# Performance work log

Measured on AMD Instinct MI355X. Metric: run time of the kernel, lower is better.

Reference implementation:

```python
import jax, jax.numpy as jnp
import numpy as np

DIM = 256
HEADS = 8


def setup_inputs() -> dict:
    key = jax.random.key(0)
    ks = jax.random.split(key, 12)
    B, N, L, C, H = 2, 1024, 4096, DIM, HEADS
    s = C ** -0.5
    inp = {
        "query": jax.random.normal(ks[0], (B, N, C), jnp.float32),
        "key": jax.random.normal(ks[1], (B, L, C), jnp.float32),
        "value": jax.random.normal(ks[2], (B, L, C), jnp.float32),
        "key_padding_mask": jnp.zeros((B, L), jnp.bool_),
        "hw_lvl": 1,
        # nn.Linear weights, stored as (out, in) like torch
        "Wq": jax.random.normal(ks[3], (C, C), jnp.float32) * s,
        "Wk": jax.random.normal(ks[4], (C, C), jnp.float32) * s,
        "Wv": jax.random.normal(ks[5], (C, C), jnp.float32) * s,
        "Wp": jax.random.normal(ks[6], (C, C), jnp.float32) * s,
        "bp": jax.random.normal(ks[7], (C,), jnp.float32) * 0.02,
        "W1": jax.random.normal(ks[8], (H, H), jnp.float32) * H ** -0.5,
        "b1": jax.random.normal(ks[9], (H,), jnp.float32) * 0.02,
        "W2": jax.random.normal(ks[10], (1, H), jnp.float32) * H ** -0.5,
        "b2": jax.random.normal(ks[11], (1,), jnp.float32) * 0.02,
    }
    return inp


def reference(query, key, value, key_padding_mask, hw_lvl,
              Wq, Wk, Wv, Wp, bp, W1, b1, W2, b2):
    # key_padding_mask and hw_lvl are accepted but unused by the original module.
    B, N, C = query.shape
    L = key.shape[1]
    H = W1.shape[0]
    D = C // H
    scale = D ** -0.5

    q = (query @ Wq.T).reshape(B, N, H, D)  # bnhd
    k = (key @ Wk.T).reshape(B, L, H, D)    # blhd
    v = (value @ Wv.T).reshape(B, L, H, D)  # blhd

    # raw attention scores [B, H, N, L]
    attn = jnp.einsum("bnhd,blhd->bhnl", q, k) * scale

    # per-score tiny MLP over the head axis -> mask [B, N, L, 1]
    scores_nlh = attn.transpose(0, 2, 3, 1)  # [B, N, L, H]
    new_feats = jax.nn.relu(scores_nlh @ W1.T + b1)
    mask = jax.nn.relu(new_feats @ W2.T + b2)  # [B, N, L, 1]

    a = jax.nn.softmax(attn, axis=-1)  # dropout p=0 -> identity
    x = jnp.einsum("bhnl,blhd->bnhd", a, v).reshape(B, N, C)
    x = x @ Wp.T + bp
    return x, mask
```

## Files before the change

kernel.cpp:

```cpp
#include <hip/hip_runtime.h>

typedef unsigned short u16;
typedef unsigned int u32;
typedef __attribute__((ext_vector_type(8))) short bf16x8;
typedef __attribute__((ext_vector_type(4))) short bf16x4;
typedef __attribute__((ext_vector_type(4))) float f32x4;

#define QK_SCALE 0.17677669529663687f

__device__ inline float bf2f(u16 h) {
    u32 u = ((u32)h) << 16; float f; __builtin_memcpy(&f, &u, 4); return f;
}
__device__ inline u16 f2bf(float f) {
    u32 u; __builtin_memcpy(&u, &f, 4);
    u = u + 0x7fffu + ((u >> 16) & 1u);
    return (u16)(u >> 16);
}

__global__ __launch_bounds__(256) void cvt_all_kernel(
    const float* __restrict__ q, const float* __restrict__ k,
    const float* __restrict__ v,
    const float* __restrict__ Wq, const float* __restrict__ Wk,
    const float* __restrict__ Wv, const float* __restrict__ Wp,
    u16* __restrict__ qf, u16* __restrict__ kf, u16* __restrict__ vf,
    u16* __restrict__ wqb, u16* __restrict__ wkb, u16* __restrict__ wvb,
    u16* __restrict__ wpb)
{
    const int bx = blockIdx.x;
    const float* src; u16* dst; int base;
    if (bx < 256)       { src = q;  dst = qf;  base = bx; }
    else if (bx < 1280) { src = k;  dst = kf;  base = bx - 256; }
    else if (bx < 2304) { src = v;  dst = vf;  base = bx - 1280; }
    else if (bx < 2336) { src = Wq; dst = wqb; base = bx - 2304; }
    else if (bx < 2368) { src = Wk; dst = wkb; base = bx - 2336; }
    else if (bx < 2400) { src = Wv; dst = wvb; base = bx - 2368; }
    else                { src = Wp; dst = wpb; base = bx - 2400; }
    const int i = base * 2048 + threadIdx.x * 8;
    const f32x4 a = *(const f32x4*)(src + i);
    const f32x4 b = *(const f32x4*)(src + i + 4);
    bf16x8 o;
#pragma unroll
    for (int j = 0; j < 4; ++j) {
        o[j]     = (short)f2bf(a[j]);
        o[j + 4] = (short)f2bf(b[j]);
    }
    *(bf16x8*)(dst + i) = o;
}

__global__ __launch_bounds__(256) void proj_kernel(
    const u16* __restrict__ qf, const u16* __restrict__ kf,
    const u16* __restrict__ vf,
    const u16* __restrict__ wqb, const u16* __restrict__ wkb,
    const u16* __restrict__ wvb,
    u16* __restrict__ qb, u16* __restrict__ kb, u16* __restrict__ vt)
{
    const int bx = blockIdx.x;
    const u16 *X, *W; u16* outb; int m0, mode;
    if (bx < 128)      { X = qf; W = wqb; outb = qb; m0 = bx * 16; mode = 2; }
    else if (bx < 640) { X = kf; W = wkb; outb = kb; m0 = (bx - 128) * 16; mode = 0; }
    else               { X = vf; W = wvb; outb = vt; m0 = (bx - 640) * 16; mode = 1; }

    const int lane = threadIdx.x & 63;
    const int w = threadIdx.x >> 6;
    const int r = lane & 15, g = lane >> 4;
    const int c0 = blockIdx.y * 64 + w * 16;
    const u16* ap = X + (long)(m0 + r) * 256 + g * 8;
    const u16* bp = W + (long)(c0 + r) * 256 + g * 8;

    bf16x8 af[8], bf[8];
#pragma unroll
    for (int ks = 0; ks < 8; ++ks) af[ks] = *(const bf16x8*)(ap + ks * 32);
#pragma unroll
    for (int ks = 0; ks < 8; ++ks) bf[ks] = *(const bf16x8*)(bp + ks * 32);

    f32x4 acc = {0.f, 0.f, 0.f, 0.f};
#pragma unroll
    for (int ks = 0; ks < 8; ++ks)
        acc = __builtin_amdgcn_mfma_f32_16x16x32_bf16(af[ks], bf[ks], acc, 0, 0, 0);

    const int c = c0 + r;
    if (mode == 1) {
        const int m_ = m0 + g * 4;
        const int b = m_ >> 12, l = m_ & 4095;
        bf16x4 pk;
#pragma unroll
        for (int j = 0; j < 4; ++j) pk[j] = (short)f2bf(acc[j]);
        *(bf16x4*)(vt + (long)b * 1048576 + (long)(l >> 2) * 1024 + c * 4) = pk;
    } else {
#pragma unroll
        for (int j = 0; j < 4; ++j) {
            const int m = m0 + g * 4 + j;
            if (mode == 2) outb[(long)m * 256 + c] = f2bf(acc[j] * QK_SCALE);
            else           outb[(long)m * 256 + c] = f2bf(acc[j]);
        }
    }
}

__global__ __launch_bounds__(256, 2) void attn_split_kernel(
    const u16* __restrict__ qb, const u16* __restrict__ kb,
    const u16* __restrict__ vt,
    const float* __restrict__ W1, const float* __restrict__ b1,
    const float* __restrict__ W2, const float* __restrict__ b2,
    u16* __restrict__ Opart, float* __restrict__ stats,
    float* __restrict__ out)
{
    __shared__ float ored[4][8][2][2][16][4];
    __shared__ float rs[4][8][16];

    const int tid = threadIdx.x;
    const int w = tid >> 6, lane = tid & 63;
    const int r = lane & 15, g = lane >> 4;
    const int bid = blockIdx.x;
    const int cz = bid & 7;
    const int bi = bid >> 9;
    const int n0 = ((bid >> 3) & 63) * 16;

    float w1r[64], b1r[8], w2r[8];
#pragma unroll
    for (int i = 0; i < 64; ++i) w1r[i] = W1[i];
#pragma unroll
    for (int i = 0; i < 8; ++i) { b1r[i] = b1[i]; w2r[i] = W2[i]; }
    const float b2r = b2[0];

    bf16x8 qh[8];
    const long qbase = (long)(bi * 1024 + n0 + r) * 256 + g * 8;
#pragma unroll
    for (int h = 0; h < 8; ++h)
        qh[h] = *(const bf16x8*)(qb + qbase + h * 32);

    f32x4 oacc[8][2];
#pragma unroll
    for (int h = 0; h < 8; ++h)
#pragma unroll
        for (int c = 0; c < 2; ++c) oacc[h][c] = (f32x4){0.f, 0.f, 0.f, 0.f};
    float rsum[8];
#pragma unroll
    for (int h = 0; h < 8; ++h) rsum[h] = 0.f;

    bf16x8 kf[8];
    {
        const long kbb = (long)(bi * 4096 + cz * 512 + w * 16 + r) * 256 + g * 8;
#pragma unroll
        for (int h = 0; h < 8; ++h)
            kf[h] = *(const bf16x8*)(kb + kbb + h * 32);
    }

    for (int t = 0; t < 8; ++t) {
        const int l0 = cz * 512 + t * 64;

        f32x4 ss[8];
#pragma unroll
        for (int h = 0; h < 8; ++h) {
            f32x4 z = {0.f, 0.f, 0.f, 0.f};
            ss[h] = __builtin_amdgcn_mfma_f32_16x16x32_bf16(kf[h], qh[h], z, 0, 0, 0);
        }

        if (t < 7) {
            const long kbb = (long)(bi * 4096 + l0 + 64 + w * 16 + r) * 256 + g * 8;
#pragma unroll
            for (int h = 0; h < 8; ++h)
                kf[h] = *(const bf16x8*)(kb + kbb + h * 32);
        }

        bf16x4 vf[8][2];
        {
            const u16* vb = vt + (long)bi * 1048576 +
                            (long)((l0 >> 2) + w * 4 + g) * 1024;
#pragma unroll
            for (int h = 0; h < 8; ++h)
#pragma unroll
                for (int c = 0; c < 2; ++c)
                    vf[h][c] = *(const bf16x4*)(vb + (h * 32 + c * 16 + r) * 4);
        }

        {
            f32x4 mv4;
#pragma unroll
            for (int j = 0; j < 4; ++j) {
                float mv = b2r;
#pragma unroll
                for (int f = 0; f < 8; ++f) {
                    float ft = b1r[f];
#pragma unroll
                    for (int h = 0; h < 8; ++h)
                        ft = fmaf(ss[h][j], w1r[f * 8 + h], ft);
                    mv = fmaf(fmaxf(ft, 0.f), w2r[f], mv);
                }
                mv4[j] = fmaxf(mv, 0.f);
            }
            *(f32x4*)(out + 524288l + (long)(bi * 1024 + n0 + r) * 4096
                      + l0 + w * 16 + g * 4) = mv4;
        }

        bf16x4 pa[8];
#pragma unroll
        for (int h = 0; h < 8; ++h) {
            float e0 = __expf(ss[h][0] - 8.f);
            float e1 = __expf(ss[h][1] - 8.f);
            float e2 = __expf(ss[h][2] - 8.f);
            float e3 = __expf(ss[h][3] - 8.f);
            rsum[h] += (e0 + e1) + (e2 + e3);
            u32 u0, u1, u2, u3;
            __builtin_memcpy(&u0, &e0, 4); __builtin_memcpy(&u1, &e1, 4);
            __builtin_memcpy(&u2, &e2, 4); __builtin_memcpy(&u3, &e3, 4);
            u32 lohi[2];
            lohi[0] = (u0 >> 16) | (u1 & 0xFFFF0000u);
            lohi[1] = (u2 >> 16) | (u3 & 0xFFFF0000u);
            __builtin_memcpy(&pa[h], lohi, 8);
        }

#pragma unroll
        for (int h = 0; h < 8; ++h)
#pragma unroll
            for (int c = 0; c < 2; ++c)
                oacc[h][c] = __builtin_amdgcn_mfma_f32_16x16x16bf16_1k(
                    pa[h], vf[h][c], oacc[h][c], 0, 0, 0);
    }

#pragma unroll
    for (int h = 0; h < 8; ++h) {
        float v = rsum[h];
        v += __shfl_xor(v, 16);
        v += __shfl_xor(v, 32);
        if (g == 0) rs[w][h][r] = v;
    }
#pragma unroll
    for (int ph = 0; ph < 2; ++ph) {
        if ((g >> 1) == ph) {
#pragma unroll
            for (int h = 0; h < 8; ++h)
#pragma unroll
                for (int c = 0; c < 2; ++c)
                    *(f32x4*)&ored[w][h][c][g & 1][r][0] = oacc[h][c];
        }
        __syncthreads();
        if (ph == 0 && tid < 128) {
            const int h = tid >> 4, n = tid & 15;
            stats[((long)(bi * 8 + cz) * 8 + h) * 1024 + n0 + n] =
                rs[0][h][n] + rs[1][h][n] + rs[2][h][n] + rs[3][h][n];
        }
        {
            const int h = tid >> 5, c = (tid >> 4) & 1, rr = tid & 15;
#pragma unroll
            for (int g2 = 0; g2 < 2; ++g2)
#pragma unroll
                for (int j = 0; j < 4; ++j) {
                    const float val =
                        ored[0][h][c][g2][rr][j] + ored[1][h][c][g2][rr][j] +
                        ored[2][h][c][g2][rr][j] + ored[3][h][c][g2][rr][j];
                    const int n = (ph * 2 + g2) * 4 + j;
                    Opart[((long)(bi * 8 + cz) * 1024 + n0 + n) * 256
                          + h * 32 + c * 16 + rr] = f2bf(val);
                }
        }
        if (ph == 0) __syncthreads();
    }
}

__global__ __launch_bounds__(512) void reduce_kernel(
    const u16* __restrict__ Opart, const float* __restrict__ stats,
    const u16* __restrict__ wpb, const float* __restrict__ bp,
    float* __restrict__ out)
{
    __shared__ __align__(16) u16 xt[16 * 272];
    const int tid = threadIdx.x;
    const int bi = blockIdx.y, n0 = blockIdx.x * 16, bz = blockIdx.z;

    {
        const int n = tid >> 5, cg = tid & 31, h = cg >> 2;
        float S = 0.f, O[8];
#pragma unroll
        for (int k = 0; k < 8; ++k) O[k] = 0.f;
#pragma unroll
        for (int c = 0; c < 8; ++c) {
            S += stats[((long)(bi * 8 + c) * 8 + h) * 1024 + n0 + n];
            bf16x8 v0 = *(const bf16x8*)(Opart +
                ((long)(bi * 8 + c) * 1024 + n0 + n) * 256 + cg * 8);
#pragma unroll
            for (int k = 0; k < 8; ++k) O[k] += bf2f((u16)v0[k]);
        }
        const float inv = 1.f / S;
        bf16x8 pk;
#pragma unroll
        for (int k = 0; k < 8; ++k) pk[k] = (short)f2bf(O[k] * inv);
        *(bf16x8*)(&xt[n * 272 + cg * 8]) = pk;
    }
    __syncthreads();

    const int w = tid >> 6, lane = tid & 63;
    const int r = lane & 15, g = lane >> 4;
    bf16x8 a8[8];
#pragma unroll
    for (int ks = 0; ks < 8; ++ks)
        a8[ks] = *(const bf16x8*)(&xt[r * 272 + ks * 32 + g * 8]);
    const int cp0 = (bz * 8 + w) * 16;
    f32x4 acc = {0.f, 0.f, 0.f, 0.f};
#pragma unroll
    for (int ks = 0; ks < 8; ++ks) {
        bf16x8 wb = *(const bf16x8*)(wpb + (long)(cp0 + r) * 256 + ks * 32 + g * 8);
        acc = __builtin_amdgcn_mfma_f32_16x16x32_bf16(a8[ks], wb, acc, 0, 0, 0);
    }
    const int cp = cp0 + r;
    const float bpv = bp[cp];
#pragma unroll
    for (int j = 0; j < 4; ++j) {
        const int nn = g * 4 + j;
        out[(long)(bi * 1024 + n0 + nn) * 256 + cp] = acc[j] + bpv;
    }
}

extern "C" void kernel_launch(void* const* d_in, const int* in_sizes, int n_in,
                              void* d_out, int out_size, void* d_ws, size_t ws_size,
                              hipStream_t stream)
{
    const float* query = (const float*)d_in[0];
    const float* key   = (const float*)d_in[1];
    const float* value = (const float*)d_in[2];
    const float* Wq = (const float*)d_in[5];
    const float* Wk = (const float*)d_in[6];
    const float* Wv = (const float*)d_in[7];
    const float* Wp = (const float*)d_in[8];
    const float* bp = (const float*)d_in[9];
    const float* W1 = (const float*)d_in[10];
    const float* b1 = (const float*)d_in[11];
    const float* W2 = (const float*)d_in[12];
    const float* b2 = (const float*)d_in[13];

    u16* qb    = (u16*)d_ws;
    u16* kb    = qb + 524288;
    u16* vtp   = kb + 2097152;
    u16* wpb   = vtp + 2097152;
    u16* Opart = wpb + 65536;
    u16* kfb   = Opart;
    u16* vfb   = Opart + 2097152;
    float* stats = (float*)(Opart + 4194304);
    u16* qfb   = (u16*)(stats + 131072);
    u16* wqb   = qfb + 524288;
    u16* wkb   = wqb + 65536;
    u16* wvb   = wkb + 65536;
    float* out = (float*)d_out;

    cvt_all_kernel<<<2432, 256, 0, stream>>>(
        query, key, value, Wq, Wk, Wv, Wp,
        qfb, kfb, vfb, wqb, wkb, wvb, wpb);
    proj_kernel<<<dim3(1152, 4), 256, 0, stream>>>(
        qfb, kfb, vfb, wqb, wkb, wvb, qb, kb, vtp);
    attn_split_kernel<<<dim3(1024), 256, 0, stream>>>(
        qb, kb, vtp, W1, b1, W2, b2, Opart, stats, out);
    reduce_kernel<<<dim3(64, 2, 2), 512, 0, stream>>>(Opart, stats, wpb, bp, out);
}
```

Before: 108.5 us.

## Fuse fp32-to-bf16 conversion into projection kernel with LDS-staged tiles

Removes the separate conversion kernel and converts query/key/value rows and weight tiles to bf16 directly into shared memory inside the projection kernel. Each block now loops over all four 64-column output chunks instead of using a 2D grid, and the Wp conversion is folded into extra blocks. This removes one launch and the bf16 intermediate write/read, at the cost of every block re-converting the full fp32 weight matrix and adding barrier-synchronized LDS staging.

```diff
diff --git a/kernel.cpp b/kernel.cpp
--- a/kernel.cpp
+++ b/kernel.cpp
@@ -7,6 +7,7 @@
 typedef __attribute__((ext_vector_type(4))) float f32x4;
 
 #define QK_SCALE 0.17677669529663687f
+#define PST 272
 
 __device__ inline float bf2f(u16 h) {
     u32 u = ((u32)h) << 16; float f; __builtin_memcpy(&f, &u, 4); return f;
@@ -16,82 +17,82 @@
     u = u + 0x7fffu + ((u >> 16) & 1u);
     return (u16)(u >> 16);
 }
-
-__global__ __launch_bounds__(256) void cvt_all_kernel(
-    const float* __restrict__ q, const float* __restrict__ k,
-    const float* __restrict__ v,
+__device__ inline bf16x8 cvt8(const float* __restrict__ p) {
+    bf16x8 o;
+#pragma unroll
+    for (int i = 0; i < 8; ++i) o[i] = (short)f2bf(p[i]);
+    return o;
+}
+
+__global__ __launch_bounds__(256) void projf_kernel(
+    const float* __restrict__ query, const float* __restrict__ key,
+    const float* __restrict__ value,
     const float* __restrict__ Wq, const float* __restrict__ Wk,
     const float* __restrict__ Wv, const float* __restrict__ Wp,
-    u16* __restrict__ qf, u16* __restrict__ kf, u16* __restrict__ vf,
-    u16* __restrict__ wqb, u16* __restrict__ wkb, u16* __restrict__ wvb,
+    u16* __restrict__ qb, u16* __restrict__ kb, u16* __restrict__ vt,
     u16* __restrict__ wpb)
 {
     const int bx = blockIdx.x;
-    const float* src; u16* dst; int base;
-    if (bx < 256)       { src = q;  dst = qf;  base = bx; }
-    else if (bx < 1280) { src = k;  dst = kf;  base = bx - 256; }
-    else if (bx < 2304) { src = v;  dst = vf;  base = bx - 1280; }
-    else if (bx < 2336) { src = Wq; dst = wqb; base = bx - 2304; }
-    else if (bx < 2368) { src = Wk; dst = wkb; base = bx - 2336; }
-    else if (bx < 2400) { src = Wv; dst = wvb; base = bx - 2368; }
-    else                { src = Wp; dst = wpb; base = bx - 2400; }
-    const int i = base * 2048 + threadIdx.x * 8;
-    const f32x4 a = *(const f32x4*)(src + i);
-    const f32x4 b = *(const f32x4*)(src + i + 4);
-    bf16x8 o;
-#pragma unroll
-    for (int j = 0; j < 4; ++j) {
-        o[j]     = (short)f2bf(a[j]);
-        o[j + 4] = (short)f2bf(b[j]);
-    }
-    *(bf16x8*)(dst + i) = o;
-}
-
-__global__ __launch_bounds__(256) void proj_kernel(
-    const u16* __restrict__ qf, const u16* __restrict__ kf,
-    const u16* __restrict__ vf,
-    const u16* __restrict__ wqb, const u16* __restrict__ wkb,
-    const u16* __restrict__ wvb,
-    u16* __restrict__ qb, u16* __restrict__ kb, u16* __restrict__ vt)
-{
-    const int bx = blockIdx.x;
-    const u16 *X, *W; u16* outb; int m0, mode;
-    if (bx < 128)      { X = qf; W = wqb; outb = qb; m0 = bx * 16; mode = 2; }
-    else if (bx < 640) { X = kf; W = wkb; outb = kb; m0 = (bx - 128) * 16; mode = 0; }
-    else               { X = vf; W = wvb; outb = vt; m0 = (bx - 640) * 16; mode = 1; }
-
-    const int lane = threadIdx.x & 63;
-    const int w = threadIdx.x >> 6;
+    const int tid = threadIdx.x;
+    if (bx >= 1152) {
+        const int idx = (bx - 1152) * 2048 + tid * 8;
+        *(bf16x8*)(wpb + idx) = cvt8(Wp + idx);
+        return;
+    }
+    const float *X, *W; u16* outb; int m0, mode;
+    if (bx < 128)      { X = query; W = Wq; outb = qb; m0 = bx * 16; mode = 2; }
+    else if (bx < 640) { X = key;   W = Wk; outb = kb; m0 = (bx - 128) * 16; mode = 0; }
+    else               { X = value; W = Wv; outb = vt; m0 = (bx - 640) * 16; mode = 1; }
+
+    __shared__ __align__(16) u16 xs[16 * PST];
+    __shared__ __align__(16) u16 ws[64 * PST];
+
+    {
+        const int row = tid >> 4, col = (tid & 15) * 16;
+        const float* src = X + (long)(m0 + row) * 256 + col;
+        *(bf16x8*)(&xs[row * PST + col])     = cvt8(src);
+        *(bf16x8*)(&xs[row * PST + col + 8]) = cvt8(src + 8);
+    }
+
+    const int lane = tid & 63, w = tid >> 6;
     const int r = lane & 15, g = lane >> 4;
-    const int c0 = blockIdx.y * 64 + w * 16;
-    const u16* ap = X + (long)(m0 + r) * 256 + g * 8;
-    const u16* bp = W + (long)(c0 + r) * 256 + g * 8;
-
-    bf16x8 af[8], bf[8];
-#pragma unroll
-    for (int ks = 0; ks < 8; ++ks) af[ks] = *(const bf16x8*)(ap + ks * 32);
-#pragma unroll
-    for (int ks = 0; ks < 8; ++ks) bf[ks] = *(const bf16x8*)(bp + ks * 32);
-
-    f32x4 acc = {0.f, 0.f, 0.f, 0.f};
-#pragma unroll
-    for (int ks = 0; ks < 8; ++ks)
-        acc = __builtin_amdgcn_mfma_f32_16x16x32_bf16(af[ks], bf[ks], acc, 0, 0, 0);
-
-    const int c = c0 + r;
-    if (mode == 1) {
-        const int m_ = m0 + g * 4;
-        const int b = m_ >> 12, l = m_ & 4095;
-        bf16x4 pk;
-#pragma unroll
-        for (int j = 0; j < 4; ++j) pk[j] = (short)f2bf(acc[j]);
-        *(bf16x4*)(vt + (long)b * 1048576 + (long)(l >> 2) * 1024 + c * 4) = pk;
-    } else {
-#pragma unroll
-        for (int j = 0; j < 4; ++j) {
-            const int m = m0 + g * 4 + j;
-            if (mode == 2) outb[(long)m * 256 + c] = f2bf(acc[j] * QK_SCALE);
-            else           outb[(long)m * 256 + c] = f2bf(acc[j]);
+
+    for (int by = 0; by < 4; ++by) {
+        __syncthreads();
+        {
+            const int row = tid >> 2, col = (tid & 3) * 64;
+            const float* src = W + (long)(by * 64 + row) * 256 + col;
+#pragma unroll
+            for (int s = 0; s < 4; ++s) {
+                *(bf16x8*)(&ws[row * PST + col + s * 16])     = cvt8(src + s * 16);
+                *(bf16x8*)(&ws[row * PST + col + s * 16 + 8]) = cvt8(src + s * 16 + 8);
+            }
+        }
+        __syncthreads();
+
+        f32x4 acc = {0.f, 0.f, 0.f, 0.f};
+#pragma unroll
+        for (int ks = 0; ks < 8; ++ks) {
+            bf16x8 a = *(const bf16x8*)(&xs[r * PST + ks * 32 + g * 8]);
+            bf16x8 b = *(const bf16x8*)(&ws[(w * 16 + r) * PST + ks * 32 + g * 8]);
+            acc = __builtin_amdgcn_mfma_f32_16x16x32_bf16(a, b, acc, 0, 0, 0);
+        }
+
+        const int c = by * 64 + w * 16 + r;
+        if (mode == 1) {
+            const int m_ = m0 + g * 4;
+            const int b = m_ >> 12, l = m_ & 4095;
+            bf16x4 pk;
+#pragma unroll
+            for (int j = 0; j < 4; ++j) pk[j] = (short)f2bf(acc[j]);
+            *(bf16x4*)(vt + (long)b * 1048576 + (long)(l >> 2) * 1024 + c * 4) = pk;
+        } else {
+#pragma unroll
+            for (int j = 0; j < 4; ++j) {
+                const int m = m0 + g * 4 + j;
+                if (mode == 2) outb[(long)m * 256 + c] = f2bf(acc[j] * QK_SCALE);
+                else           outb[(long)m * 256 + c] = f2bf(acc[j]);
+            }
         }
     }
 }
@@ -331,20 +332,11 @@
     u16* vtp   = kb + 2097152;
     u16* wpb   = vtp + 2097152;
     u16* Opart = wpb + 65536;
-    u16* kfb   = Opart;
-    u16* vfb   = Opart + 2097152;
     float* stats = (float*)(Opart + 4194304);
-    u16* qfb   = (u16*)(stats + 131072);
-    u16* wqb   = qfb + 524288;
-    u16* wkb   = wqb + 65536;
-    u16* wvb   = wkb + 65536;
     float* out = (float*)d_out;
 
-    cvt_all_kernel<<<2432, 256, 0, stream>>>(
-        query, key, value, Wq, Wk, Wv, Wp,
-        qfb, kfb, vfb, wqb, wkb, wvb, wpb);
-    proj_kernel<<<dim3(1152, 4), 256, 0, stream>>>(
-        qfb, kfb, vfb, wqb, wkb, wvb, qb, kb, vtp);
+    projf_kernel<<<dim3(1184), 256, 0, stream>>>(
+        query, key, value, Wq, Wk, Wv, Wp, qb, kb, vtp, wpb);
     attn_split_kernel<<<dim3(1024), 256, 0, stream>>>(
         qb, kb, vtp, W1, b1, W2, b2, Opart, stats, out);
     reduce_kernel<<<dim3(64, 2, 2), 512, 0, stream>>>(Opart, stats, wpb, bp, out);
```

Measured after the change: 109.2 us. Within noise of the previous version (+0.7%).
